# Optimization experiments

Hardware: AMD Instinct MI355X
Metric: run time of the kernel (lower is better)

## Reference

```python
import jax, jax.numpy as jnp
import numpy as np

B, C, H, W = 16, 64, 256, 256
K = 3  # kernel_size
STRIDE = (1, 1)
PAD = ((1, 1), (1, 1))
DIL = (1, 1)


def setup_inputs() -> dict:
    key = jax.random.key(0)
    k1, k2 = jax.random.split(key)
    x = jax.random.normal(k1, (B, C, H, W), dtype=jnp.float32)
    kernel = jax.random.normal(k2, (B, K, K), dtype=jnp.float32)
    return {"x": x, "kernel": kernel}


def reference(x, kernel):
    # Original: builds [B,B,K,K] kernel, zeroes off-diagonal blocks, runs full
    # conv2d on x permuted to [C,B,H,W]. Mathematically this is a per-sample
    # depthwise conv: out[b,c] = conv2d(x[b,c], kernel[b]).
    # We honor the block-diagonal sparsity via feature_group_count=B.
    b = x.shape[0]
    xt = jnp.transpose(x, (1, 0, 2, 3))          # [C, B, H, W]: conv batch=C, channels=B
    w = kernel[:, None, :, :]                    # [B, 1, K, K] depthwise weights
    y = jax.lax.conv_general_dilated(
        xt, w,
        window_strides=STRIDE,
        padding=PAD,
        rhs_dilation=DIL,
        dimension_numbers=("NCHW", "OIHW", "NCHW"),
        feature_group_count=b,
    )                                            # [C, B, H', W']
    return jnp.transpose(y, (1, 0, 2, 3))        # [B, C, H', W']
```

## Files before the change

kernel.cpp:

```cpp
#include <hip/hip_runtime.h>
#include <hip/hip_bf16.h>


#define BB 16
#define CC 64
#define HH 256
#define WW 256

__global__ __launch_bounds__(256) void ParConv2d_dw3x3(
    const float* __restrict__ x,
    const float* __restrict__ kern,
    float* __restrict__ out)
{
    const int idx = blockIdx.x * 256 + threadIdx.x;
    const int w4 = idx & 63;
    const int h  = (idx >> 6) & 255;
    const int bc = idx >> 14;
    const int b  = bc >> 6;

    const float* kb = kern + b * 9;
    const float k00 = kb[0], k01 = kb[1], k02 = kb[2];
    const float k10 = kb[3], k11 = kb[4], k12 = kb[5];
    const float k20 = kb[6], k21 = kb[7], k22 = kb[8];

    const float* xp = x + (size_t)bc * (HH * WW);
    const int w0 = w4 << 2;

    float row[3][6];
#pragma unroll
    for (int r = 0; r < 3; ++r) {
        const int hh = h + r - 1;
        if (hh < 0 || hh >= HH) {
#pragma unroll
            for (int j = 0; j < 6; ++j) row[r][j] = 0.0f;
        } else {
            const float* rp = xp + hh * WW + w0;
            const float4 v = *(const float4*)rp;
            row[r][1] = v.x; row[r][2] = v.y; row[r][3] = v.z; row[r][4] = v.w;
            row[r][0] = (w0 > 0)        ? rp[-1] : 0.0f;
            row[r][5] = (w0 + 4 < WW)   ? rp[4]  : 0.0f;
        }
    }

    float res[4];
#pragma unroll
    for (int j = 0; j < 4; ++j) {
        res[j] = k00 * row[0][j] + k01 * row[0][j + 1] + k02 * row[0][j + 2]
               + k10 * row[1][j] + k11 * row[1][j + 1] + k12 * row[1][j + 2]
               + k20 * row[2][j] + k21 * row[2][j + 1] + k22 * row[2][j + 2];
    }

    float4* op = (float4*)(out + (size_t)idx * 4);
    *op = make_float4(res[0], res[1], res[2], res[3]);
}

extern "C" void kernel_launch(void* const* d_in, const int* in_sizes, int n_in,
                              void* d_out, int out_size, void* d_ws, size_t ws_size,
                              hipStream_t stream) {
    const float* x    = (const float*)d_in[0];
    const float* kern = (const float*)d_in[1];
    float* out        = (float*)d_out;

    const int total_threads = BB * CC * HH * (WW / 4);
    const int blocks = total_threads / 256;
    ParConv2d_dw3x3<<<blocks, 256, 0, stream>>>(x, kern, out);
}
```

Measured before the change: 503.3 us.

## Compute four output rows per thread and fetch halo columns via wave shuffles

```diff
diff --git a/kernel.cpp b/kernel.cpp
--- a/kernel.cpp
+++ b/kernel.cpp
@@ -2,7 +2,6 @@
 #include <hip/hip_bf16.h>
 
 
-#define BB 16
 #define CC 64
 #define HH 256
 #define WW 256
@@ -12,11 +11,12 @@
     const float* __restrict__ kern,
     float* __restrict__ out)
 {
-    const int idx = blockIdx.x * 256 + threadIdx.x;
-    const int w4 = idx & 63;
-    const int h  = (idx >> 6) & 255;
-    const int bc = idx >> 14;
-    const int b  = bc >> 6;
+    const int tid  = threadIdx.x;
+    const int lane = tid & 63;
+    const int wave = tid >> 6;
+    const int tile = blockIdx.x & 15;
+    const int bc   = blockIdx.x >> 4;
+    const int b    = bc >> 6;
 
     const float* kb = kern + b * 9;
     const float k00 = kb[0], k01 = kb[1], k02 = kb[2];
@@ -24,34 +24,36 @@
     const float k20 = kb[6], k21 = kb[7], k22 = kb[8];
 
     const float* xp = x + (size_t)bc * (HH * WW);
-    const int w0 = w4 << 2;
+    const int h0 = tile * 16 + wave * 4;
+    const int w0 = lane << 2;
 
-    float row[3][6];
+    float win[6][6];
 #pragma unroll
-    for (int r = 0; r < 3; ++r) {
-        const int hh = h + r - 1;
-        if (hh < 0 || hh >= HH) {
-#pragma unroll
-            for (int j = 0; j < 6; ++j) row[r][j] = 0.0f;
-        } else {
-            const float* rp = xp + hh * WW + w0;
-            const float4 v = *(const float4*)rp;
-            row[r][1] = v.x; row[r][2] = v.y; row[r][3] = v.z; row[r][4] = v.w;
-            row[r][0] = (w0 > 0)        ? rp[-1] : 0.0f;
-            row[r][5] = (w0 + 4 < WW)   ? rp[4]  : 0.0f;
+    for (int r = 0; r < 6; ++r) {
+        const int hh = h0 + r - 1;
+        float4 v = make_float4(0.f, 0.f, 0.f, 0.f);
+        if (hh >= 0 && hh < HH) {
+            v = *(const float4*)(xp + hh * WW + w0);
         }
+        const float l = __shfl_up(v.w, 1);
+        const float rr = __shfl_down(v.x, 1);
+        win[r][0] = (lane == 0)  ? 0.f : l;
+        win[r][1] = v.x; win[r][2] = v.y; win[r][3] = v.z; win[r][4] = v.w;
+        win[r][5] = (lane == 63) ? 0.f : rr;
     }
 
-    float res[4];
+    float* op = out + (size_t)bc * (HH * WW) + (size_t)h0 * WW + w0;
 #pragma unroll
-    for (int j = 0; j < 4; ++j) {
-        res[j] = k00 * row[0][j] + k01 * row[0][j + 1] + k02 * row[0][j + 2]
-               + k10 * row[1][j] + k11 * row[1][j + 1] + k12 * row[1][j + 2]
-               + k20 * row[2][j] + k21 * row[2][j + 1] + k22 * row[2][j + 2];
+    for (int orow = 0; orow < 4; ++orow) {
+        float res[4];
+#pragma unroll
+        for (int j = 0; j < 4; ++j) {
+            res[j] = k00 * win[orow][j]     + k01 * win[orow][j + 1]     + k02 * win[orow][j + 2]
+                   + k10 * win[orow + 1][j] + k11 * win[orow + 1][j + 1] + k12 * win[orow + 1][j + 2]
+                   + k20 * win[orow + 2][j] + k21 * win[orow + 2][j + 1] + k22 * win[orow + 2][j + 2];
+        }
+        *(float4*)(op + orow * WW) = make_float4(res[0], res[1], res[2], res[3]);
     }
-
-    float4* op = (float4*)(out + (size_t)idx * 4);
-    *op = make_float4(res[0], res[1], res[2], res[3]);
 }
 
 extern "C" void kernel_launch(void* const* d_in, const int* in_sizes, int n_in,
@@ -61,7 +63,6 @@
     const float* kern = (const float*)d_in[1];
     float* out        = (float*)d_out;
 
-    const int total_threads = BB * CC * HH * (WW / 4);
-    const int blocks = total_threads / 256;
+    const int blocks = 16 * CC * 16;
     ParConv2d_dw3x3<<<blocks, 256, 0, stream>>>(x, kern, out);
 }
```

Result: faster. 430.1 us (-14.6%).
